# Kernel tuning notes

Hardware: AMD Instinct MI355X
Metric: run time of the kernel (lower is better)

The kernel has to match this reference:

```python
import jax, jax.numpy as jnp
import numpy as np

POOL = 7  # pool_size = (7, 7)


def setup_inputs() -> dict:
    key = jax.random.key(0)
    k1, k2, k3 = jax.random.split(key, 3)
    B, H, W, C = 1, 128, 128, 512
    N = 1024
    feature_maps = jax.random.normal(k1, (B, H, W, C), dtype=jnp.float32)
    # rois = (x1, y1, x2, y2) int coords, guaranteed x2 > x1, y2 > y1 (min size 8)
    xy1 = jax.random.randint(k2, (N, 2), 0, W - 8)
    wh = jax.random.randint(k3, (N, 2), 8, 64)
    x2 = jnp.minimum(xy1[:, 0] + wh[:, 0], W)
    y2 = jnp.minimum(xy1[:, 1] + wh[:, 1], H)
    rois = jnp.stack([xy1[:, 0], xy1[:, 1], x2, y2], axis=1).astype(jnp.int32)
    return {"feature_maps": feature_maps, "rois": rois}


def _half_pixel_coords(start, size, out_size):
    # tf.image.resize (TF2 bilinear) uses half-pixel centers:
    #   src = (dst + 0.5) * (in / out) - 0.5, clamped to [0, in-1]
    sizef = size.astype(jnp.float32)
    scale = sizef / out_size
    c = (jnp.arange(out_size, dtype=jnp.float32) + 0.5) * scale - 0.5
    c = jnp.clip(c, 0.0, sizef - 1.0)
    return c + start.astype(jnp.float32)


def reference(feature_maps, rois):
    # feature_maps: [B, H, W, C]; rois: [N, 4] int (x1, y1, x2, y2)
    def pool_one(roi):
        x1, y1, x2, y2 = roi[0], roi[1], roi[2], roi[3]
        ys = _half_pixel_coords(y1, y2 - y1, POOL)  # [7] absolute y coords
        xs = _half_pixel_coords(x1, x2 - x1, POOL)  # [7] absolute x coords
        y0 = jnp.floor(ys).astype(jnp.int32)
        x0 = jnp.floor(xs).astype(jnp.int32)
        y1i = jnp.minimum(y0 + 1, y2 - 1)  # clamp within crop (edge replicate)
        x1i = jnp.minimum(x0 + 1, x2 - 1)
        wy = (ys - y0.astype(jnp.float32))[None, :, None, None]
        wx = (xs - x0.astype(jnp.float32))[None, None, :, None]
        tl = feature_maps[:, y0[:, None], x0[None, :], :]   # [B,7,7,C]
        tr = feature_maps[:, y0[:, None], x1i[None, :], :]
        bl = feature_maps[:, y1i[:, None], x0[None, :], :]
        br = feature_maps[:, y1i[:, None], x1i[None, :], :]
        top = tl + (tr - tl) * wx
        bot = bl + (br - bl) * wx
        return top + (bot - top) * wy  # [B, 7, 7, C]

    # tf.map_fn over rois stacks per-roi results -> [N, B, 7, 7, C]
    return jax.vmap(pool_one)(rois)
```

## Files before the change

kernel.cpp:

```cpp
#include <hip/hip_runtime.h>


#define POOLN 7
#define FM_H 128
#define FM_W 128
#define FM_C 512
#define NXCD 8
#define CHUNK_C (FM_C / NXCD)
#define BINS_PER_BLOCK 16

typedef float f32x4 __attribute__((ext_vector_type(4)));

__global__ __launch_bounds__(256) void roi_align_kernel(
    const float* __restrict__ fm,
    const int* __restrict__ rois,
    float* __restrict__ out,
    int n_bins)
{
    const int chunk  = blockIdx.x & (NXCD - 1);
    const int group  = blockIdx.x >> 3;
    const int lane_c = threadIdx.x & 15;
    const int bin    = group * BINS_PER_BLOCK + (threadIdx.x >> 4);
    if (bin >= n_bins) return;

    const int roi = bin / 49;
    const int rem = bin - roi * 49;
    const int py  = rem / 7;
    const int px  = rem - py * 7;

    const int4 r = reinterpret_cast<const int4*>(rois)[roi];
    const int x1 = r.x, y1 = r.y, x2 = r.z, y2 = r.w;

    const float sizy = (float)(y2 - y1);
    float cy = ((float)py + 0.5f) * (sizy / (float)POOLN) - 0.5f;
    cy = fminf(fmaxf(cy, 0.0f), sizy - 1.0f);
    const float ys = cy + (float)y1;
    const int   y0 = (int)floorf(ys);
    const int   yb = min(y0 + 1, y2 - 1);
    const float wy = ys - (float)y0;

    const float sizx = (float)(x2 - x1);
    float cx = ((float)px + 0.5f) * (sizx / (float)POOLN) - 0.5f;
    cx = fminf(fmaxf(cx, 0.0f), sizx - 1.0f);
    const float xs = cx + (float)x1;
    const int   x0 = (int)floorf(xs);
    const int   xb = min(x0 + 1, x2 - 1);
    const float wx = xs - (float)x0;

    const int coff = chunk * CHUNK_C + lane_c * 4;

    const f32x4 a = *reinterpret_cast<const f32x4*>(fm + (size_t)(y0 * FM_W + x0) * FM_C + coff);
    const f32x4 b = *reinterpret_cast<const f32x4*>(fm + (size_t)(y0 * FM_W + xb) * FM_C + coff);
    const f32x4 d = *reinterpret_cast<const f32x4*>(fm + (size_t)(yb * FM_W + x0) * FM_C + coff);
    const f32x4 e = *reinterpret_cast<const f32x4*>(fm + (size_t)(yb * FM_W + xb) * FM_C + coff);

    const f32x4 top = a + (b - a) * wx;
    const f32x4 bot = d + (e - d) * wx;
    const f32x4 res = top + (bot - top) * wy;

    f32x4* o = reinterpret_cast<f32x4*>(out + (size_t)bin * FM_C + coff);
    __builtin_nontemporal_store(res, o);
}

extern "C" void kernel_launch(void* const* d_in, const int* in_sizes, int n_in,
                              void* d_out, int out_size, void* d_ws, size_t ws_size,
                              hipStream_t stream) {
    const float* fm   = (const float*)d_in[0];
    const int*   rois = (const int*)d_in[1];
    float*       out  = (float*)d_out;

    const int N      = in_sizes[1] / 4;
    const int n_bins = N * POOLN * POOLN;
    const int groups = (n_bins + BINS_PER_BLOCK - 1) / BINS_PER_BLOCK;
    dim3 grid(groups * NXCD);
    roi_align_kernel<<<grid, 256, 0, stream>>>(fm, rois, out, n_bins);
}
```

Before: 30.85 us.

## Use persistent grid-stride blocks with software-pipelined prefetch of next bin

Replaces the one-bin-per-thread launch with a fixed grid of 2048 blocks. Each thread walks bins with a grid stride and loads the four corner vectors for the next bin before it interpolates and stores the current one. The aim is to overlap gather latency with compute and store, and to cut block launch overhead. In exchange it uses more registers and has fewer waves resident to hide latency. Offsets are now 32-bit ints, which is fine for this feature-map size.

New measurement: 32.35 us. +4.9%, slower.

```diff
diff --git a/kernel.cpp b/kernel.cpp
--- a/kernel.cpp
+++ b/kernel.cpp
@@ -2,12 +2,13 @@
 
 
 #define POOLN 7
-#define FM_H 128
 #define FM_W 128
 #define FM_C 512
 #define NXCD 8
-#define CHUNK_C (FM_C / NXCD)
-#define BINS_PER_BLOCK 16
+#define CHUNK_C 64
+#define BINS_PER_ITER 16
+#define NGROUPS 256
+#define STRIDE (BINS_PER_ITER * NGROUPS)
 
 typedef float f32x4 __attribute__((ext_vector_type(4)));
 
@@ -17,49 +18,78 @@
     float* __restrict__ out,
     int n_bins)
 {
-    const int chunk  = blockIdx.x & (NXCD - 1);
-    const int group  = blockIdx.x >> 3;
-    const int lane_c = threadIdx.x & 15;
-    const int bin    = group * BINS_PER_BLOCK + (threadIdx.x >> 4);
-    if (bin >= n_bins) return;
+    const int chunk = blockIdx.x & (NXCD - 1);
+    const int group = blockIdx.x >> 3;
+    const int lane  = threadIdx.x & 15;
+    const int sub   = threadIdx.x >> 4;
+    const int coff  = chunk * CHUNK_C + lane * 4;
 
-    const int roi = bin / 49;
-    const int rem = bin - roi * 49;
-    const int py  = rem / 7;
-    const int px  = rem - py * 7;
+    auto coords = [&](int b, int& oa, int& ob, int& od, int& oe,
+                      float& wxo, float& wyo) {
+        const int roi = b / 49;
+        const int rem = b - roi * 49;
+        const int py  = rem / 7;
+        const int px  = rem - py * 7;
 
-    const int4 r = reinterpret_cast<const int4*>(rois)[roi];
-    const int x1 = r.x, y1 = r.y, x2 = r.z, y2 = r.w;
+        const int4 r = reinterpret_cast<const int4*>(rois)[roi];
+        const int x1 = r.x, y1 = r.y, x2 = r.z, y2 = r.w;
 
-    const float sizy = (float)(y2 - y1);
-    float cy = ((float)py + 0.5f) * (sizy / (float)POOLN) - 0.5f;
-    cy = fminf(fmaxf(cy, 0.0f), sizy - 1.0f);
-    const float ys = cy + (float)y1;
-    const int   y0 = (int)floorf(ys);
-    const int   yb = min(y0 + 1, y2 - 1);
-    const float wy = ys - (float)y0;
+        const float sizy = (float)(y2 - y1);
+        float cy = ((float)py + 0.5f) * (sizy / (float)POOLN) - 0.5f;
+        cy = fminf(fmaxf(cy, 0.0f), sizy - 1.0f);
+        const float ys = cy + (float)y1;
+        const int   y0 = (int)floorf(ys);
+        const int   yb = min(y0 + 1, y2 - 1);
+        wyo = ys - (float)y0;
 
-    const float sizx = (float)(x2 - x1);
-    float cx = ((float)px + 0.5f) * (sizx / (float)POOLN) - 0.5f;
-    cx = fminf(fmaxf(cx, 0.0f), sizx - 1.0f);
-    const float xs = cx + (float)x1;
-    const int   x0 = (int)floorf(xs);
-    const int   xb = min(x0 + 1, x2 - 1);
-    const float wx = xs - (float)x0;
+        const float sizx = (float)(x2 - x1);
+        float cx = ((float)px + 0.5f) * (sizx / (float)POOLN) - 0.5f;
+        cx = fminf(fmaxf(cx, 0.0f), sizx - 1.0f);
+        const float xs = cx + (float)x1;
+        const int   x0 = (int)floorf(xs);
+        const int   xb = min(x0 + 1, x2 - 1);
+        wxo = xs - (float)x0;
 
-    const int coff = chunk * CHUNK_C + lane_c * 4;
+        oa = (y0 * FM_W + x0) * FM_C + coff;
+        ob = (y0 * FM_W + xb) * FM_C + coff;
+        od = (yb * FM_W + x0) * FM_C + coff;
+        oe = (yb * FM_W + xb) * FM_C + coff;
+    };
 
-    const f32x4 a = *reinterpret_cast<const f32x4*>(fm + (size_t)(y0 * FM_W + x0) * FM_C + coff);
-    const f32x4 b = *reinterpret_cast<const f32x4*>(fm + (size_t)(y0 * FM_W + xb) * FM_C + coff);
-    const f32x4 d = *reinterpret_cast<const f32x4*>(fm + (size_t)(yb * FM_W + x0) * FM_C + coff);
-    const f32x4 e = *reinterpret_cast<const f32x4*>(fm + (size_t)(yb * FM_W + xb) * FM_C + coff);
+    int bin = group * BINS_PER_ITER + sub;
+    int oa, ob, od, oe;
+    float wx, wy;
+    coords(bin, oa, ob, od, oe, wx, wy);
+    f32x4 a  = *reinterpret_cast<const f32x4*>(fm + oa);
+    f32x4 bb = *reinterpret_cast<const f32x4*>(fm + ob);
+    f32x4 d  = *reinterpret_cast<const f32x4*>(fm + od);
+    f32x4 e  = *reinterpret_cast<const f32x4*>(fm + oe);
 
-    const f32x4 top = a + (b - a) * wx;
-    const f32x4 bot = d + (e - d) * wx;
-    const f32x4 res = top + (bot - top) * wy;
+    for (;;) {
+        const int nbin = bin + STRIDE;
+        const bool nv = nbin < n_bins;
 
-    f32x4* o = reinterpret_cast<f32x4*>(out + (size_t)bin * FM_C + coff);
-    __builtin_nontemporal_store(res, o);
+        f32x4 na, nb, nd, ne;
+        float nwx = 0.f, nwy = 0.f;
+        if (nv) {
+            int qa, qb, qd, qe;
+            coords(nbin, qa, qb, qd, qe, nwx, nwy);
+            na = *reinterpret_cast<const f32x4*>(fm + qa);
+            nb = *reinterpret_cast<const f32x4*>(fm + qb);
+            nd = *reinterpret_cast<const f32x4*>(fm + qd);
+            ne = *reinterpret_cast<const f32x4*>(fm + qe);
+        }
+
+        const f32x4 top = a + (bb - a) * wx;
+        const f32x4 bot = d + (e - d) * wx;
+        const f32x4 res = top + (bot - top) * wy;
+        f32x4* o = reinterpret_cast<f32x4*>(out + (size_t)bin * FM_C + coff);
+        __builtin_nontemporal_store(res, o);
+
+        if (!nv) break;
+        bin = nbin; wx = nwx; wy = nwy;
+        a = na; bb = nb; d = nd; e = ne;
+    }
 }
 
 extern "C" void kernel_launch(void* const* d_in, const int* in_sizes, int n_in,
@@ -71,7 +101,6 @@
 
     const int N      = in_sizes[1] / 4;
     const int n_bins = N * POOLN * POOLN;
-    const int groups = (n_bins + BINS_PER_BLOCK - 1) / BINS_PER_BLOCK;
-    dim3 grid(groups * NXCD);
+    dim3 grid(NGROUPS * NXCD);
     roi_align_kernel<<<grid, 256, 0, stream>>>(fm, rois, out, n_bins);
 }
```
